# Kernel optimization log

Measured on AMD Instinct MI355X. Metric: run time of the kernel, lower is better.

## Reference

```python
import jax, jax.numpy as jnp
import numpy as np

K = 8        # neighborhood kernel size (ksize)
HEADS = 8
GROUPS = 32  # GroupNorm groups
EPS = 1e-6
DIL = 1      # dilation


def _nbr_idx(L, k, d):
    # NATTEN-style neighborhood: fixed-size window, shifted (clamped) at borders
    span = (k - 1) * d + 1
    i = jnp.arange(L)
    start = jnp.clip(i - ((k - 1) // 2) * d, 0, L - span)
    return start[:, None] + jnp.arange(k)[None, :] * d  # [L, k]


def _group_norm(x, gamma, beta):
    B, C, H, W = x.shape
    xg = x.reshape(B, GROUPS, C // GROUPS, H, W)
    mu = xg.mean(axis=(2, 3, 4), keepdims=True)
    var = xg.var(axis=(2, 3, 4), keepdims=True)
    xn = ((xg - mu) * jax.lax.rsqrt(var + EPS)).reshape(B, C, H, W)
    return xn * gamma[None, :, None, None] + beta[None, :, None, None]


def setup_inputs() -> dict:
    key = jax.random.key(0)
    ks = jax.random.split(key, 4)
    B, C, H, W = 2, 128, 96, 96
    x = jax.random.normal(ks[0], (B, C, H, W), dtype=jnp.float32)
    gn_gamma = jnp.ones((C,), jnp.float32)
    gn_beta = jnp.zeros((C,), jnp.float32)
    qkv_w = jax.random.normal(ks[1], (3 * C, C), dtype=jnp.float32) * (C ** -0.5)
    qkv_b = jnp.zeros((3 * C,), jnp.float32)
    proj_w = jax.random.normal(ks[2], (C, C), dtype=jnp.float32) * (C ** -0.5)
    proj_b = jnp.zeros((C,), jnp.float32)
    return {"x": x, "gn_gamma": gn_gamma, "gn_beta": gn_beta,
            "qkv_w": qkv_w, "qkv_b": qkv_b, "proj_w": proj_w, "proj_b": proj_b}


def reference(x, gn_gamma, gn_beta, qkv_w, qkv_b, proj_w, proj_b):
    B, C, H, W = x.shape
    hd = C // HEADS
    h = _group_norm(x, gn_gamma, gn_beta)
    # 1x1 conv -> qkv
    qkv = jnp.einsum('bchw,oc->bohw', h, qkv_w) + qkv_b[None, :, None, None]
    # 'b (qkv h c) x y -> qkv b x y h c'
    qkv = qkv.reshape(B, 3, HEADS, hd, H, W).transpose(1, 0, 4, 5, 2, 3)
    q, k, v = qkv[0], qkv[1], qkv[2]  # [B,H,W,heads,hd]

    ih = _nbr_idx(H, K, DIL)  # [H,K]
    iw = _nbr_idx(W, K, DIL)  # [W,K]
    # gather per-pixel K x K neighborhoods -> [B,H,W,K,K,heads,hd]
    k_win = k[:, ih[:, None, :, None], iw[None, :, None, :]]
    v_win = v[:, ih[:, None, :, None], iw[None, :, None, :]]

    scale = np.float32(1.0 / np.sqrt(hd))
    logits = jnp.einsum('bxyhc,bxyijhc->bxyhij', q * scale, k_win)
    logits = logits.reshape(B, H, W, HEADS, K * K)
    attn = jax.nn.softmax(logits, axis=-1)
    out = jnp.einsum('bxyhm,bxymhc->bxyhc', attn,
                     v_win.reshape(B, H, W, K * K, HEADS, hd))
    # 'b x y h c -> b (h c) x y'
    out = out.transpose(0, 3, 4, 1, 2).reshape(B, C, H, W)
    return jnp.einsum('bchw,oc->bohw', out, proj_w) + proj_b[None, :, None, None]
```

## Files before the change

### kernel.cpp

```cpp
#include <hip/hip_runtime.h>
#include <hip/hip_bf16.h>

typedef unsigned short u16;
typedef unsigned int   u32;
typedef __attribute__((ext_vector_type(8))) short short8;
typedef __attribute__((ext_vector_type(4))) float f32x4;

#define BATCH 2
#define CCH   128
#define HH    96
#define WW    96
#define HWSZ  9216
#define HEADS 8
#define HD    16
#define GROUPS 32
#define EPSV  1e-6f

static __device__ __forceinline__ u16 f2bf(float f) {
    u32 u = __builtin_bit_cast(u32, f);
    u = (u + 0x7FFFu + ((u >> 16) & 1u)) >> 16;
    return (u16)u;
}
static __device__ __forceinline__ short8 mk8(u32 a, u32 b, u32 c, u32 d) {
    union { short8 v; u32 w[4]; } u; u.w[0]=a; u.w[1]=b; u.w[2]=c; u.w[3]=d; return u.v;
}

__global__ __launch_bounds__(256) void gn_wpack(const float* __restrict__ x,
                                                float* __restrict__ partial,
                                                const float* __restrict__ qkv_w,
                                                const float* __restrict__ proj_w,
                                                u16* __restrict__ Wq, u16* __restrict__ Wp) {
    if (blockIdx.x < 256) {
        const int bq = blockIdx.x;
        const float4* base = (const float4*)(x + (size_t)bq * 9216);
        float s = 0.f, ss = 0.f;
        #pragma unroll
        for (int i = 0; i < 9; ++i) {
            float4 v = base[threadIdx.x + i * 256];
            s  += v.x + v.y + v.z + v.w;
            ss += v.x * v.x + v.y * v.y + v.z * v.z + v.w * v.w;
        }
        #pragma unroll
        for (int off = 32; off > 0; off >>= 1) {
            s  += __shfl_down(s, off);
            ss += __shfl_down(ss, off);
        }
        __shared__ float rs[4], rss[4];
        const int wid = threadIdx.x >> 6, lane = threadIdx.x & 63;
        if (lane == 0) { rs[wid] = s; rss[wid] = ss; }
        __syncthreads();
        if (threadIdx.x == 0) {
            partial[2 * bq]     = rs[0] + rs[1] + rs[2] + rs[3];
            partial[2 * bq + 1] = rss[0] + rss[1] + rss[2] + rss[3];
        }
    } else {
        const int t = (blockIdx.x - 256) * 256 + threadIdx.x;
        if (t < 16 * 384) {
            int cb = t / 384, o = t % 384;
            u16 pk[8];
            #pragma unroll
            for (int j = 0; j < 8; ++j) pk[j] = f2bf(qkv_w[o * 128 + cb * 8 + j]);
            uint4 r;
            r.x = (u32)pk[0] | ((u32)pk[1] << 16); r.y = (u32)pk[2] | ((u32)pk[3] << 16);
            r.z = (u32)pk[4] | ((u32)pk[5] << 16); r.w = (u32)pk[6] | ((u32)pk[7] << 16);
            *(uint4*)(Wq + (size_t)t * 8) = r;
        } else if (t < 16 * 384 + 16 * 128) {
            int i = t - 16 * 384;
            int cb = i / 128, o = i % 128;
            u16 pk[8];
            #pragma unroll
            for (int j = 0; j < 8; ++j) pk[j] = f2bf(proj_w[o * 128 + cb * 8 + j]);
            uint4 r;
            r.x = (u32)pk[0] | ((u32)pk[1] << 16); r.y = (u32)pk[2] | ((u32)pk[3] << 16);
            r.z = (u32)pk[4] | ((u32)pk[5] << 16); r.w = (u32)pk[6] | ((u32)pk[7] << 16);
            *(uint4*)(Wp + (size_t)i * 8) = r;
        }
    }
}

__global__ __launch_bounds__(256) void qkv_fused(const float* __restrict__ x,
                                                 const float* __restrict__ partial,
                                                 const float* __restrict__ gamma,
                                                 const float* __restrict__ beta,
                                                 const u16* __restrict__ Wq,
                                                 const float* __restrict__ qkv_b,
                                                 u16* __restrict__ qkvp,
                                                 u16* __restrict__ vT) {
    __shared__ float scale[CCH], shift[CCH];
    __shared__ u16 smem[128 * 136];
    const int t = threadIdx.x;
    const int pph = blockIdx.x;
    const int L = (pph & 7) * 54 + (pph >> 3);
    const int b = L / 216;
    const int r = L % 216;
    const int pt = r / 3, ot = r % 3;

    if (t < CCH) {
        const int c = t, g = c >> 2, bg = b * GROUPS + g;
        float S = 0.f, SS = 0.f;
        #pragma unroll
        for (int q = 0; q < 4; ++q) {
            S  += partial[2 * (bg * 4 + q)];
            SS += partial[2 * (bg * 4 + q) + 1];
        }
        const float mean = S * (1.f / 36864.f);
        const float rstd = rsqrtf(SS * (1.f / 36864.f) - mean * mean + EPSV);
        const float sc = rstd * gamma[c];
        scale[c] = sc;
        shift[c] = beta[c] - mean * sc;
    }
    __syncthreads();

    {
        const int px = t & 127, chh = t >> 7;
        const float* xb = x + (size_t)b * CCH * HWSZ + (size_t)pt * 128 + px;
        #pragma unroll
        for (int cbi = 0; cbi < 8; ++cbi) {
            const int cb = chh * 8 + cbi;
            u16 pk[8];
            #pragma unroll
            for (int j = 0; j < 8; ++j) {
                const int c = cb * 8 + j;
                pk[j] = f2bf(xb[(size_t)c * HWSZ] * scale[c] + shift[c]);
            }
            uint4 o;
            o.x = (u32)pk[0] | ((u32)pk[1] << 16);
            o.y = (u32)pk[2] | ((u32)pk[3] << 16);
            o.z = (u32)pk[4] | ((u32)pk[5] << 16);
            o.w = (u32)pk[6] | ((u32)pk[7] << 16);
            *(uint4*)&smem[((size_t)cb * 128 + px) * 8] = o;
        }
    }
    __syncthreads();

    const int l = t & 63, w = t >> 6;
    const int OB = ot * 128 + (w & 1) * 64;
    const int PL = (w >> 1) * 64;
    const int q = l >> 4, lo = l & 15;

    float bv[4][4];
    #pragma unroll
    for (int of = 0; of < 4; ++of)
        #pragma unroll
        for (int r2 = 0; r2 < 4; ++r2) bv[of][r2] = qkv_b[OB + of * 16 + q * 4 + r2];

    f32x4 acc[4][4] = {};
    #pragma unroll
    for (int ks = 0; ks < 4; ++ks) {
        const int cb = ks * 4 + q;
        short8 a[4];
        #pragma unroll
        for (int of = 0; of < 4; ++of)
            a[of] = *(const short8*)(Wq + ((size_t)cb * 384 + OB + of * 16 + lo) * 8);
        #pragma unroll
        for (int pf = 0; pf < 4; ++pf) {
            short8 bb = *(const short8*)&smem[((size_t)cb * 128 + PL + pf * 16 + lo) * 8];
            #pragma unroll
            for (int of = 0; of < 4; ++of)
                acc[of][pf] = __builtin_amdgcn_mfma_f32_16x16x32_bf16(a[of], bb, acc[of][pf], 0, 0, 0);
        }
    }

    if (ot < 2) {
        #pragma unroll
        for (int of = 0; of < 4; ++of) {
            const int plane = b * 16 + (OB >> 4) + of;
            #pragma unroll
            for (int pf = 0; pf < 4; ++pf) {
                const int p = pt * 128 + PL + pf * 16 + lo;
                u16 h0 = f2bf(acc[of][pf][0] + bv[of][0]);
                u16 h1 = f2bf(acc[of][pf][1] + bv[of][1]);
                u16 h2 = f2bf(acc[of][pf][2] + bv[of][2]);
                u16 h3 = f2bf(acc[of][pf][3] + bv[of][3]);
                uint2 pkt;
                pkt.x = (u32)h0 | ((u32)h1 << 16);
                pkt.y = (u32)h2 | ((u32)h3 << 16);
                *(uint2*)(qkvp + ((size_t)plane * HWSZ + p) * 16 + q * 4) = pkt;
            }
        }
    } else {
        __syncthreads();
        #pragma unroll
        for (int of = 0; of < 4; ++of) {
            const int orow = (OB - 256) + of * 16 + q * 4;
            #pragma unroll
            for (int pf = 0; pf < 4; ++pf) {
                const int px = PL + pf * 16 + lo;
                #pragma unroll
                for (int r2 = 0; r2 < 4; ++r2)
                    smem[(orow + r2) * 136 + px] = f2bf(acc[of][pf][r2] + bv[of][r2]);
            }
        }
        __syncthreads();
        #pragma unroll
        for (int k = 0; k < 8; ++k) {
            const int idx = t + k * 256;
            const int row = idx >> 4, px8 = idx & 15;
            const int h = row >> 4, ch = row & 15;
            uint4 v = *(const uint4*)&smem[row * 136 + px8 * 8];
            *(uint4*)(vT + ((((size_t)(b * 8 + h)) * 16 + ch) * HWSZ)
                      + (size_t)pt * 128 + px8 * 8) = v;
        }
    }
}

__global__ __launch_bounds__(256) void proj_gemm(const u16* __restrict__ Wpk,
                                                 const u16* __restrict__ Xpk,
                                                 const float* __restrict__ bias,
                                                 float* __restrict__ out_f32) {
    const int bid = blockIdx.x;
    const int b = bid / 144, pt = bid % 144;
    const int l = threadIdx.x & 63, w = threadIdx.x >> 6;
    const int OB = (w & 1) * 64;
    const int PB = pt * 64 + (w >> 1) * 32;
    const int q = l >> 4, lo = l & 15;
    const u16* Xb = Xpk + (size_t)b * 16 * HWSZ * 8;

    float bv[4][4];
    #pragma unroll
    for (int of = 0; of < 4; ++of)
        #pragma unroll
        for (int r = 0; r < 4; ++r) bv[of][r] = bias[OB + of * 16 + q * 4 + r];

    f32x4 acc[4][2] = {};
    #pragma unroll
    for (int ks = 0; ks < 4; ++ks) {
        const int cb = ks * 4 + q;
        short8 a[4];
        #pragma unroll
        for (int of = 0; of < 4; ++of)
            a[of] = *(const short8*)(Wpk + ((size_t)cb * 128 + OB + of * 16 + lo) * 8);
        #pragma unroll
        for (int pf = 0; pf < 2; ++pf) {
            short8 bb = *(const short8*)(Xb + ((size_t)cb * HWSZ + PB + pf * 16 + lo) * 8);
            #pragma unroll
            for (int of = 0; of < 4; ++of)
                acc[of][pf] = __builtin_amdgcn_mfma_f32_16x16x32_bf16(a[of], bb, acc[of][pf], 0, 0, 0);
        }
    }

    #pragma unroll
    for (int of = 0; of < 4; ++of) {
        #pragma unroll
        for (int pf = 0; pf < 2; ++pf) {
            const int p = PB + pf * 16 + lo;
            #pragma unroll
            for (int r = 0; r < 4; ++r) {
                const int o = OB + of * 16 + q * 4 + r;
                out_f32[((size_t)(b * 128 + o)) * HWSZ + p] = acc[of][pf][r] + bv[of][r];
            }
        }
    }
}

__global__ __launch_bounds__(384) void natten_mfma(const u16* __restrict__ qkv,
                                                   const u16* __restrict__ vT,
                                                   u16* __restrict__ attn_out) {
    __shared__ u16 Ks[13 * 64 * 16];
    __shared__ u16 VsT[16 * 840];
    const int tid = threadIdx.x;
    const int xh = blockIdx.x & 1, yb = blockIdx.x >> 1;
    const int h = blockIdx.y, b = blockIdx.z;
    const int ry0 = min(max(yb * 6 - 3, 0), 83);
    const int rx0 = xh * 32;

    for (int i = tid; i < 3328; i += 384) {
        if (i < 1664) {
            const int px = i >> 1, half = i & 1;
            const int row = px >> 6, col = px & 63;
            const u16* gp = qkv + ((size_t)(b * 16 + 8 + h) * HWSZ
                                 + (ry0 + row) * WW + rx0 + col) * 16 + half * 8;
            *(uint4*)&Ks[px * 16 + half * 8] = *(const uint4*)gp;
        } else {
            const int j2 = i - 1664;
            const int ch = j2 / 104, r2 = j2 - ch * 104;
            const int row = r2 >> 3, c8 = r2 & 7;
            const u16* gp = vT + (((size_t)(b * 8 + h)) * 16 + ch) * HWSZ
                               + (ry0 + row) * WW + rx0 + c8 * 8;
            *(uint4*)&VsT[ch * 840 + row * 64 + c8 * 8] = *(const uint4*)gp;
        }
    }
    __syncthreads();

    const int l = tid & 63, wv = tid >> 6;
    const int m = l & 15, q4 = l >> 4;
    const int yq = m >> 3, xq = m & 7;

    for (int j = 0; j < 3; ++j) {
        const int g = wv * 3 + j;
        const int gy = g / 6, gx = g % 6;
        const int y0g = yb * 6 + gy * 2, x0g = xh * 48 + gx * 8;
        const int yabs = y0g + yq, xabs = x0g + xq;
        const int sy = min(max(yabs - 3, 0), 88);
        const int sx = min(max(xabs - 3, 0), 88);
        const int dy0 = min(max(y0g - 3, 0), 88) - ry0;
        const int rd0 = dy0 - (sy - ry0);
        const int cx0 = (min(max(x0g - 3 - rx0, 0), 48)) & ~3;
        const int cd0 = cx0 + q4 * 4 - (sx - rx0);
        const int qpix = yabs * WW + xabs;

        const uint2 qw = *(const uint2*)(qkv + ((size_t)(b * 16 + h) * HWSZ + qpix) * 16 + q4 * 4);
        const short8 qb = mk8(qw.x, qw.y, 0u, 0u);

        float ev[9][4];
        float vs = 0.f;
        #pragma unroll
        for (int t = 0; t < 9; ++t) {
            const int trow = min(dy0 + t, 12);
            const uint2 kk = *(const uint2*)&Ks[(trow * 64 + cx0 + m) * 16 + q4 * 4];
            f32x4 lg = __builtin_amdgcn_mfma_f32_16x16x32_bf16(
                mk8(kk.x, kk.y, kk.x, kk.y), qb, (f32x4){0.f, 0.f, 0.f, 0.f}, 0, 0, 0);
            const bool rv = (u32)(t + rd0) < 8u;
            #pragma unroll
            for (int r = 0; r < 4; ++r) {
                const bool ok = rv && ((u32)(cd0 + r) < 8u);
                const float e = ok ? __expf(lg[r] * 0.25f) : 0.f;
                ev[t][r] = e;
                vs += e;
            }
        }
        vs += __shfl_xor(vs, 16);
        vs += __shfl_xor(vs, 32);
        const float inv = 1.0f / vs;

        u32 pd0[9], pd1[9];
        #pragma unroll
        for (int t = 0; t < 9; ++t) {
            pd0[t] = (u32)f2bf(ev[t][0] * inv) | ((u32)f2bf(ev[t][1] * inv) << 16);
            pd1[t] = (u32)f2bf(ev[t][2] * inv) | ((u32)f2bf(ev[t][3] * inv) << 16);
        }

        f32x4 acc = {};
        #pragma unroll
        for (int t = 0; t < 9; ++t) {
            const int trow = min(dy0 + t, 12);
            const uint2 va = *(const uint2*)&VsT[m * 840 + trow * 64 + cx0 + q4 * 4];
            acc = __builtin_amdgcn_mfma_f32_16x16x32_bf16(
                mk8(va.x, va.y, va.x, va.y), mk8(pd0[t], pd1[t], 0u, 0u), acc, 0, 0, 0);
        }

        uint2 od;
        od.x = (u32)f2bf(acc[0]) | ((u32)f2bf(acc[1]) << 16);
        od.y = (u32)f2bf(acc[2]) | ((u32)f2bf(acc[3]) << 16);
        *(uint2*)(attn_out + ((size_t)(b * 16 + h * 2 + (q4 >> 1)) * HWSZ + qpix) * 8
                  + (q4 & 1) * 4) = od;
    }
}

extern "C" void kernel_launch(void* const* d_in, const int* in_sizes, int n_in,
                              void* d_out, int out_size, void* d_ws, size_t ws_size,
                              hipStream_t stream) {
    const float* x      = (const float*)d_in[0];
    const float* gamma  = (const float*)d_in[1];
    const float* beta   = (const float*)d_in[2];
    const float* qkv_w  = (const float*)d_in[3];
    const float* qkv_b  = (const float*)d_in[4];
    const float* proj_w = (const float*)d_in[5];
    const float* proj_b = (const float*)d_in[6];
    float* out = (float*)d_out;

    char* wsb = (char*)d_ws;
    float* partial = (float*)wsb;
    u16* Wq    = (u16*)(wsb + 4096);
    u16* Wp    = Wq + 16 * 384 * 8;
    u16* qkvp  = Wp + 16 * 128 * 8;
    u16* vT    = qkvp + (size_t)BATCH * 16 * HWSZ * HD;
    u16* attnp = vT + (size_t)BATCH * 8 * HD * HWSZ;

    gn_wpack<<<288, 256, 0, stream>>>(x, partial, qkv_w, proj_w, Wq, Wp);

    qkv_fused<<<432, 256, 0, stream>>>(x, partial, gamma, beta, Wq, qkv_b, qkvp, vT);

    natten_mfma<<<dim3(32, HEADS, BATCH), 384, 0, stream>>>(qkvp, vT, attnp);

    proj_gemm<<<288, 256, 0, stream>>>(Wp, attnp, proj_b, out);
}
```

Before: 43.15 us.

## Store V pixel-major like Q/K and transpose into LDS inside attention kernel

The QKV kernel now writes V in the same pixel-major packed layout as Q and K, which removes its separate LDS transpose path and extra barriers. The attention kernel transposes V while loading it into shared memory, using scalar 16-bit LDS stores. Softmax masking now adds a large negative bias inside the exponent instead of using branches, and normalisation is applied once to the output accumulator instead of to every probability. bf16 conversion uses the native __bf16 cast, which gives fewer conversion instructions but adds scattered LDS writes in the attention load phase.

```diff
diff --git a/kernel.cpp b/kernel.cpp
--- a/kernel.cpp
+++ b/kernel.cpp
@@ -17,9 +17,10 @@
 #define EPSV  1e-6f
 
 static __device__ __forceinline__ u16 f2bf(float f) {
-    u32 u = __builtin_bit_cast(u32, f);
-    u = (u + 0x7FFFu + ((u >> 16) & 1u)) >> 16;
-    return (u16)u;
+    return __builtin_bit_cast(u16, (__bf16)f);
+}
+static __device__ __forceinline__ u32 pk2(float a, float b) {
+    return (u32)f2bf(a) | ((u32)f2bf(b) << 16);
 }
 static __device__ __forceinline__ short8 mk8(u32 a, u32 b, u32 c, u32 d) {
     union { short8 v; u32 w[4]; } u; u.w[0]=a; u.w[1]=b; u.w[2]=c; u.w[3]=d; return u.v;
@@ -84,10 +85,9 @@
                                                  const float* __restrict__ beta,
                                                  const u16* __restrict__ Wq,
                                                  const float* __restrict__ qkv_b,
-                                                 u16* __restrict__ qkvp,
-                                                 u16* __restrict__ vT) {
+                                                 u16* __restrict__ qkvp) {
     __shared__ float scale[CCH], shift[CCH];
-    __shared__ u16 smem[128 * 136];
+    __shared__ u16 Xt[16 * 128 * 8];
     const int t = threadIdx.x;
     const int pph = blockIdx.x;
     const int L = (pph & 7) * 54 + (pph >> 3);
@@ -121,14 +121,14 @@
             #pragma unroll
             for (int j = 0; j < 8; ++j) {
                 const int c = cb * 8 + j;
-                pk[j] = f2bf(xb[(size_t)c * HWSZ] * scale[c] + shift[c]);
+                pk[j] = f2bf(__builtin_fmaf(xb[(size_t)c * HWSZ], scale[c], shift[c]));
             }
             uint4 o;
             o.x = (u32)pk[0] | ((u32)pk[1] << 16);
             o.y = (u32)pk[2] | ((u32)pk[3] << 16);
             o.z = (u32)pk[4] | ((u32)pk[5] << 16);
             o.w = (u32)pk[6] | ((u32)pk[7] << 16);
-            *(uint4*)&smem[((size_t)cb * 128 + px) * 8] = o;
+            *(uint4*)&Xt[((size_t)cb * 128 + px) * 8] = o;
         }
     }
     __syncthreads();
@@ -154,52 +154,23 @@
             a[of] = *(const short8*)(Wq + ((size_t)cb * 384 + OB + of * 16 + lo) * 8);
         #pragma unroll
         for (int pf = 0; pf < 4; ++pf) {
-            short8 bb = *(const short8*)&smem[((size_t)cb * 128 + PL + pf * 16 + lo) * 8];
+            short8 bb = *(const short8*)&Xt[((size_t)cb * 128 + PL + pf * 16 + lo) * 8];
             #pragma unroll
             for (int of = 0; of < 4; ++of)
                 acc[of][pf] = __builtin_amdgcn_mfma_f32_16x16x32_bf16(a[of], bb, acc[of][pf], 0, 0, 0);
         }
     }
 
-    if (ot < 2) {
-        #pragma unroll
-        for (int of = 0; of < 4; ++of) {
-            const int plane = b * 16 + (OB >> 4) + of;
-            #pragma unroll
-            for (int pf = 0; pf < 4; ++pf) {
-                const int p = pt * 128 + PL + pf * 16 + lo;
-                u16 h0 = f2bf(acc[of][pf][0] + bv[of][0]);
-                u16 h1 = f2bf(acc[of][pf][1] + bv[of][1]);
-                u16 h2 = f2bf(acc[of][pf][2] + bv[of][2]);
-                u16 h3 = f2bf(acc[of][pf][3] + bv[of][3]);
-                uint2 pkt;
-                pkt.x = (u32)h0 | ((u32)h1 << 16);
-                pkt.y = (u32)h2 | ((u32)h3 << 16);
-                *(uint2*)(qkvp + ((size_t)plane * HWSZ + p) * 16 + q * 4) = pkt;
-            }
-        }
-    } else {
-        __syncthreads();
-        #pragma unroll
-        for (int of = 0; of < 4; ++of) {
-            const int orow = (OB - 256) + of * 16 + q * 4;
-            #pragma unroll
-            for (int pf = 0; pf < 4; ++pf) {
-                const int px = PL + pf * 16 + lo;
-                #pragma unroll
-                for (int r2 = 0; r2 < 4; ++r2)
-                    smem[(orow + r2) * 136 + px] = f2bf(acc[of][pf][r2] + bv[of][r2]);
-            }
-        }
-        __syncthreads();
-        #pragma unroll
-        for (int k = 0; k < 8; ++k) {
-            const int idx = t + k * 256;
-            const int row = idx >> 4, px8 = idx & 15;
-            const int h = row >> 4, ch = row & 15;
-            uint4 v = *(const uint4*)&smem[row * 136 + px8 * 8];
-            *(uint4*)(vT + ((((size_t)(b * 8 + h)) * 16 + ch) * HWSZ)
-                      + (size_t)pt * 128 + px8 * 8) = v;
+    #pragma unroll
+    for (int of = 0; of < 4; ++of) {
+        const int plane = b * 24 + (OB >> 4) + of;
+        #pragma unroll
+        for (int pf = 0; pf < 4; ++pf) {
+            const int p = pt * 128 + PL + pf * 16 + lo;
+            uint2 pkt;
+            pkt.x = pk2(acc[of][pf][0] + bv[of][0], acc[of][pf][1] + bv[of][1]);
+            pkt.y = pk2(acc[of][pf][2] + bv[of][2], acc[of][pf][3] + bv[of][3]);
+            *(uint2*)(qkvp + ((size_t)plane * HWSZ + p) * 16 + q * 4) = pkt;
         }
     }
 }
@@ -254,7 +225,6 @@
 }
 
 __global__ __launch_bounds__(384) void natten_mfma(const u16* __restrict__ qkv,
-                                                   const u16* __restrict__ vT,
                                                    u16* __restrict__ attn_out) {
     __shared__ u16 Ks[13 * 64 * 16];
     __shared__ u16 VsT[16 * 840];
@@ -268,16 +238,25 @@
         if (i < 1664) {
             const int px = i >> 1, half = i & 1;
             const int row = px >> 6, col = px & 63;
-            const u16* gp = qkv + ((size_t)(b * 16 + 8 + h) * HWSZ
+            const u16* gp = qkv + ((size_t)(b * 24 + 8 + h) * HWSZ
                                  + (ry0 + row) * WW + rx0 + col) * 16 + half * 8;
             *(uint4*)&Ks[px * 16 + half * 8] = *(const uint4*)gp;
         } else {
             const int j2 = i - 1664;
-            const int ch = j2 / 104, r2 = j2 - ch * 104;
-            const int row = r2 >> 3, c8 = r2 & 7;
-            const u16* gp = vT + (((size_t)(b * 8 + h)) * 16 + ch) * HWSZ
-                               + (ry0 + row) * WW + rx0 + c8 * 8;
-            *(uint4*)&VsT[ch * 840 + row * 64 + c8 * 8] = *(const uint4*)gp;
+            const int px = j2 >> 1, half = j2 & 1;
+            const int row = px >> 6, col = px & 63;
+            const u16* gp = qkv + ((size_t)(b * 24 + 16 + h) * HWSZ
+                                 + (ry0 + row) * WW + rx0 + col) * 16 + half * 8;
+            const uint4 vv = *(const uint4*)gp;
+            const int ch0 = half * 8;
+            VsT[(ch0 + 0) * 840 + px] = (u16)(vv.x);
+            VsT[(ch0 + 1) * 840 + px] = (u16)(vv.x >> 16);
+            VsT[(ch0 + 2) * 840 + px] = (u16)(vv.y);
+            VsT[(ch0 + 3) * 840 + px] = (u16)(vv.y >> 16);
+            VsT[(ch0 + 4) * 840 + px] = (u16)(vv.z);
+            VsT[(ch0 + 5) * 840 + px] = (u16)(vv.z >> 16);
+            VsT[(ch0 + 6) * 840 + px] = (u16)(vv.w);
+            VsT[(ch0 + 7) * 840 + px] = (u16)(vv.w >> 16);
         }
     }
     __syncthreads();
@@ -299,8 +278,13 @@
         const int cd0 = cx0 + q4 * 4 - (sx - rx0);
         const int qpix = yabs * WW + xabs;
 
-        const uint2 qw = *(const uint2*)(qkv + ((size_t)(b * 16 + h) * HWSZ + qpix) * 16 + q4 * 4);
+        const uint2 qw = *(const uint2*)(qkv + ((size_t)(b * 24 + h) * HWSZ + qpix) * 16 + q4 * 4);
         const short8 qb = mk8(qw.x, qw.y, 0u, 0u);
+
+        const float NEGB = -1e30f;
+        float colb[4];
+        #pragma unroll
+        for (int r = 0; r < 4; ++r) colb[r] = ((u32)(cd0 + r) < 8u) ? 0.f : NEGB;
 
         float ev[9][4];
         float vs = 0.f;
@@ -310,11 +294,10 @@
             const uint2 kk = *(const uint2*)&Ks[(trow * 64 + cx0 + m) * 16 + q4 * 4];
             f32x4 lg = __builtin_amdgcn_mfma_f32_16x16x32_bf16(
                 mk8(kk.x, kk.y, kk.x, kk.y), qb, (f32x4){0.f, 0.f, 0.f, 0.f}, 0, 0, 0);
-            const bool rv = (u32)(t + rd0) < 8u;
+            const float rb = ((u32)(t + rd0) < 8u) ? 0.f : NEGB;
             #pragma unroll
             for (int r = 0; r < 4; ++r) {
-                const bool ok = rv && ((u32)(cd0 + r) < 8u);
-                const float e = ok ? __expf(lg[r] * 0.25f) : 0.f;
+                const float e = __expf(__builtin_fmaf(lg[r], 0.25f, colb[r] + rb));
                 ev[t][r] = e;
                 vs += e;
             }
@@ -326,8 +309,8 @@
         u32 pd0[9], pd1[9];
         #pragma unroll
         for (int t = 0; t < 9; ++t) {
-            pd0[t] = (u32)f2bf(ev[t][0] * inv) | ((u32)f2bf(ev[t][1] * inv) << 16);
-            pd1[t] = (u32)f2bf(ev[t][2] * inv) | ((u32)f2bf(ev[t][3] * inv) << 16);
+            pd0[t] = pk2(ev[t][0], ev[t][1]);
+            pd1[t] = pk2(ev[t][2], ev[t][3]);
         }
 
         f32x4 acc = {};
@@ -340,8 +323,8 @@
         }
 
         uint2 od;
-        od.x = (u32)f2bf(acc[0]) | ((u32)f2bf(acc[1]) << 16);
-        od.y = (u32)f2bf(acc[2]) | ((u32)f2bf(acc[3]) << 16);
+        od.x = pk2(acc[0] * inv, acc[1] * inv);
+        od.y = pk2(acc[2] * inv, acc[3] * inv);
         *(uint2*)(attn_out + ((size_t)(b * 16 + h * 2 + (q4 >> 1)) * HWSZ + qpix) * 8
                   + (q4 & 1) * 4) = od;
     }
@@ -364,14 +347,13 @@
     u16* Wq    = (u16*)(wsb + 4096);
     u16* Wp    = Wq + 16 * 384 * 8;
     u16* qkvp  = Wp + 16 * 128 * 8;
-    u16* vT    = qkvp + (size_t)BATCH * 16 * HWSZ * HD;
-    u16* attnp = vT + (size_t)BATCH * 8 * HD * HWSZ;
+    u16* attnp = qkvp + (size_t)BATCH * 24 * HWSZ * HD;
 
     gn_wpack<<<288, 256, 0, stream>>>(x, partial, qkv_w, proj_w, Wq, Wp);
 
-    qkv_fused<<<432, 256, 0, stream>>>(x, partial, gamma, beta, Wq, qkv_b, qkvp, vT);
-
-    natten_mfma<<<dim3(32, HEADS, BATCH), 384, 0, stream>>>(qkvp, vT, attnp);
+    qkv_fused<<<432, 256, 0, stream>>>(x, partial, gamma, beta, Wq, qkv_b, qkvp);
+
+    natten_mfma<<<dim3(32, HEADS, BATCH), 384, 0, stream>>>(qkvp, attnp);
 
     proj_gemm<<<288, 256, 0, stream>>>(Wp, attnp, proj_b, out);
 }
```

Result: faster. 41.68 us (-3.4%).
